# Kernel optimization log

Hardware: AMD Instinct MI355X
Metric: run time of the kernel (lower is better)

The kernel has to match this reference:

```python
import jax, jax.numpy as jnp
import numpy as np

POOL_H, POOL_W = 7, 7


def _crop_and_resize(fmap, boxes, box_idx, ph, pw):
    """TF tf.image.crop_and_resize (bilinear) for normalized boxes.
    fmap: [B,H,W,C], boxes: [M,4] (y1,x1,y2,x2), box_idx: [M] int32 -> [M,ph,pw,C]."""
    H, W = fmap.shape[1], fmap.shape[2]
    dt = fmap.dtype
    y1, x1, y2, x2 = jnp.split(boxes.astype(dt), 4, axis=1)  # each [M,1]
    gy = jnp.arange(ph, dtype=dt) / (ph - 1)
    gx = jnp.arange(pw, dtype=dt) / (pw - 1)
    ys = (y1 + (y2 - y1) * gy[None, :]) * (H - 1)  # [M,ph]
    xs = (x1 + (x2 - x1) * gx[None, :]) * (W - 1)  # [M,pw]
    y0 = jnp.clip(jnp.floor(ys), 0, H - 1).astype(jnp.int32)
    x0 = jnp.clip(jnp.floor(xs), 0, W - 1).astype(jnp.int32)
    y1i = jnp.minimum(y0 + 1, H - 1)
    x1i = jnp.minimum(x0 + 1, W - 1)
    ly = (ys - y0.astype(dt))[:, :, None, None]  # [M,ph,1,1]
    lx = (xs - x0.astype(dt))[:, None, :, None]  # [M,1,pw,1]
    b = box_idx[:, None, None]
    tl = fmap[b, y0[:, :, None], x0[:, None, :]]   # [M,ph,pw,C]
    tr = fmap[b, y0[:, :, None], x1i[:, None, :]]
    bl = fmap[b, y1i[:, :, None], x0[:, None, :]]
    br = fmap[b, y1i[:, :, None], x1i[:, None, :]]
    top = tl + (tr - tl) * lx
    bot = bl + (br - bl) * lx
    return top + (bot - top) * ly


def pyramid_roi_align(boxes, image_meta, feature_maps):
    B, N, _ = boxes.shape
    y1, x1, y2, x2 = jnp.split(boxes, 4, axis=2)
    h = y2 - y1
    w = x2 - x1
    image_shape = image_meta[0, 4:7]
    image_area = image_shape[0] * image_shape[1]
    roi_level = jnp.log2(jnp.sqrt(h * w) / (224.0 / jnp.sqrt(image_area)))
    roi_level = jnp.clip(4 + jnp.round(roi_level).astype(jnp.int32), 2, 5)
    roi_level = roi_level.reshape(B * N)  # squeeze axis 2 + flatten

    flat_boxes = boxes.reshape(B * N, 4)
    box_idx = jnp.repeat(jnp.arange(B, dtype=jnp.int32), N)
    C = feature_maps[0].shape[-1]
    pooled = jnp.zeros((B * N, POOL_H, POOL_W, C), dtype=feature_maps[0].dtype)
    # Equivalent to TF's gather/crop/sort-restore: each box pooled from its level.
    for i, level in enumerate(range(2, 6)):
        crop = _crop_and_resize(feature_maps[i], flat_boxes, box_idx, POOL_H, POOL_W)
        mask = (roi_level == level)[:, None, None, None]
        pooled = jnp.where(mask, crop, pooled)
    return pooled.reshape(B, N, POOL_H, POOL_W, C)


def setup_inputs() -> dict:
    key = jax.random.key(0)
    k1, k2, k3, k4, k5, k6, k7, k8 = jax.random.split(key, 8)
    B, N, C = 2, 1000, 256
    # boxes: normalized y1,x1,y2,x2 with sizes spanning all FPN levels
    sz = jax.random.uniform(k1, (B, N, 1), minval=0.02, maxval=0.8)
    yx1 = jax.random.uniform(k2, (B, N, 2)) * (1.0 - sz)
    boxes = jnp.concatenate([yx1[..., :1], yx1[..., 1:], yx1[..., :1] + sz, yx1[..., 1:] + sz], axis=2)
    # image_meta: image_shape (1024,1024,3) at indices 4:7
    meta = np.zeros((B, 93), dtype=np.float32)
    meta[:, 1:4] = [1024, 1024, 3]
    meta[:, 4:7] = [1024, 1024, 3]
    meta[:, 11] = 1.0
    return {
        "boxes": boxes.astype(jnp.float32),
        "image_meta": jnp.asarray(meta),
        "feat_p2": jax.random.normal(k3, (B, 256, 256, C), dtype=jnp.float32),
        "feat_p3": jax.random.normal(k4, (B, 128, 128, C), dtype=jnp.float32),
        "feat_p4": jax.random.normal(k5, (B, 64, 64, C), dtype=jnp.float32),
        "feat_p5": jax.random.normal(k6, (B, 32, 32, C), dtype=jnp.float32),
    }


def reference(boxes, image_meta, feat_p2, feat_p3, feat_p4, feat_p5):
    return pyramid_roi_align(boxes, image_meta, (feat_p2, feat_p3, feat_p4, feat_p5))
```

## Files before the change

### kernel.cpp

```cpp
#include <hip/hip_runtime.h>


__global__ __launch_bounds__(256) void roi_align_kernel(
    const float* __restrict__ boxes,
    const float* __restrict__ meta,
    const float* __restrict__ f2,
    const float* __restrict__ f3,
    const float* __restrict__ f4,
    const float* __restrict__ f5,
    float* __restrict__ out,
    int boxes_per_batch,
    long total4)
{
    long idx = (long)blockIdx.x * blockDim.x + threadIdx.x;
    if (idx >= total4) return;

    int c4  = (int)(idx & 63);
    long t  = idx >> 6;
    int p   = (int)(t % 49);
    int box = (int)(t / 49);
    int py = p / 7, px = p % 7;

    float by1 = boxes[4 * box + 0];
    float bx1 = boxes[4 * box + 1];
    float by2 = boxes[4 * box + 2];
    float bx2 = boxes[4 * box + 3];

    float h = by2 - by1, w = bx2 - bx1;
    float area  = meta[4] * meta[5];
    float scale = 224.0f / sqrtf(area);
    float rl    = log2f(sqrtf(h * w) / scale);
    int lvl = 4 + (int)rintf(rl);
    lvl = lvl < 2 ? 2 : (lvl > 5 ? 5 : lvl);
    int li = lvl - 2;
    const float* f = (li == 0) ? f2 : (li == 1) ? f3 : (li == 2) ? f4 : f5;
    int H = 256 >> li;

    int b = box / boxes_per_batch;

    float gy = (float)py / 6.0f;
    float gx = (float)px / 6.0f;
    float ys = (by1 + (by2 - by1) * gy) * (float)(H - 1);
    float xs = (bx1 + (bx2 - bx1) * gx) * (float)(H - 1);

    float fy0 = fminf(fmaxf(floorf(ys), 0.0f), (float)(H - 1));
    float fx0 = fminf(fmaxf(floorf(xs), 0.0f), (float)(H - 1));
    int y0 = (int)fy0, x0 = (int)fx0;
    int y1i = min(y0 + 1, H - 1);
    int x1i = min(x0 + 1, H - 1);
    float ly = ys - fy0;
    float lx = xs - fx0;

    const int C = 256;
    size_t row0 = ((size_t)b * H + y0)  * H;
    size_t row1 = ((size_t)b * H + y1i) * H;
    const float4* tl = (const float4*)(f + (row0 + x0)  * C) + c4;
    const float4* tr = (const float4*)(f + (row0 + x1i) * C) + c4;
    const float4* bl = (const float4*)(f + (row1 + x0)  * C) + c4;
    const float4* br = (const float4*)(f + (row1 + x1i) * C) + c4;

    float4 vtl = *tl, vtr = *tr, vbl = *bl, vbr = *br;
    float4 r;
    float top, bot;
    top = vtl.x + (vtr.x - vtl.x) * lx; bot = vbl.x + (vbr.x - vbl.x) * lx; r.x = top + (bot - top) * ly;
    top = vtl.y + (vtr.y - vtl.y) * lx; bot = vbl.y + (vbr.y - vbl.y) * lx; r.y = top + (bot - top) * ly;
    top = vtl.z + (vtr.z - vtl.z) * lx; bot = vbl.z + (vbr.z - vbl.z) * lx; r.z = top + (bot - top) * ly;
    top = vtl.w + (vtr.w - vtl.w) * lx; bot = vbl.w + (vbr.w - vbl.w) * lx; r.w = top + (bot - top) * ly;

    ((float4*)out)[idx] = r;
}

extern "C" void kernel_launch(void* const* d_in, const int* in_sizes, int n_in,
                              void* d_out, int out_size, void* d_ws, size_t ws_size,
                              hipStream_t stream) {
    const float* boxes = (const float*)d_in[0];
    const float* meta  = (const float*)d_in[1];
    const float* f2    = (const float*)d_in[2];
    const float* f3    = (const float*)d_in[3];
    const float* f4    = (const float*)d_in[4];
    const float* f5    = (const float*)d_in[5];
    float* out         = (float*)d_out;

    int n_boxes = in_sizes[0] / 4;
    int B       = in_sizes[2] / (256 * 256 * 256);
    int boxes_per_batch = n_boxes / B;

    long total4 = (long)n_boxes * 49 * 64;
    int blocks  = (int)((total4 + 255) / 256);
    roi_align_kernel<<<blocks, 256, 0, stream>>>(
        boxes, meta, f2, f3, f4, f5, out, boxes_per_batch, total4);
}
```

Measured before the change: 43.15 us.

## Split ROI align into per-box prep kernel and XCD-swizzled gather kernel

Adds a prep kernel that computes, per box, the pyramid level and the per-axis row/column offsets and interpolation weights into workspace. The gather kernel then reads these tables instead of recomputing log2/sqrt per thread. Each thread now handles two float4 channel chunks, output uses nontemporal stores, and block IDs are remapped so that contiguous work lands on the same XCD for L2 locality. The cost is an extra kernel launch and workspace traffic, and the new path depends on the workspace being large enough; otherwise it falls back to the old kernel.

```diff
diff --git a/kernel.cpp b/kernel.cpp
--- a/kernel.cpp
+++ b/kernel.cpp
@@ -1,5 +1,135 @@
 #include <hip/hip_runtime.h>
-
+#include <math.h>
+
+
+#define POOLN 7
+#define CCH 256
+
+typedef float f32x4 __attribute__((ext_vector_type(4)));
+
+struct __align__(16) AxisInfo { int r0; int r1; float l; int pad; };
+
+__global__ __launch_bounds__(64) void roi_prep_kernel(
+    const float* __restrict__ boxes,
+    const float* __restrict__ meta,
+    int* __restrict__ liArr,
+    AxisInfo* __restrict__ yinfo,
+    AxisInfo* __restrict__ xinfo,
+    int n_boxes, int boxes_per_batch)
+{
+    int tid = blockIdx.x * blockDim.x + threadIdx.x;
+    int box = tid / POOLN;
+    int j   = tid - box * POOLN;
+    if (box >= n_boxes) return;
+
+    float by1 = boxes[4 * box + 0];
+    float bx1 = boxes[4 * box + 1];
+    float by2 = boxes[4 * box + 2];
+    float bx2 = boxes[4 * box + 3];
+    float h = by2 - by1, w = bx2 - bx1;
+
+    float area  = meta[4] * meta[5];
+    float scale = 224.0f / sqrtf(area);
+    float rl    = log2f(sqrtf(h * w) / scale);
+    int lvl = 4 + (int)rintf(rl);
+    lvl = lvl < 2 ? 2 : (lvl > 5 ? 5 : lvl);
+    int li = lvl - 2;
+    int H  = 256 >> li;
+    if (j == 0) liArr[box] = li;
+
+    int b = box / boxes_per_batch;
+    float g = (float)j / 6.0f;
+    float hm1 = (float)(H - 1);
+
+    float ys  = (by1 + h * g) * hm1;
+    float fy0 = fminf(fmaxf(floorf(ys), 0.0f), hm1);
+    int y0  = (int)fy0;
+    int y1i = min(y0 + 1, H - 1);
+    AxisInfo yi;
+    yi.r0 = ((b * H + y0)  * H) * CCH;
+    yi.r1 = ((b * H + y1i) * H) * CCH;
+    yi.l  = ys - fy0;
+    yi.pad = 0;
+    yinfo[box * POOLN + j] = yi;
+
+    float xs  = (bx1 + w * g) * hm1;
+    float fx0 = fminf(fmaxf(floorf(xs), 0.0f), hm1);
+    int x0  = (int)fx0;
+    int x1i = min(x0 + 1, H - 1);
+    AxisInfo xi;
+    xi.r0 = x0  * CCH;
+    xi.r1 = x1i * CCH;
+    xi.l  = xs - fx0;
+    xi.pad = 0;
+    xinfo[box * POOLN + j] = xi;
+}
+
+__device__ __forceinline__ f32x4 bilerp4(f32x4 tl, f32x4 tr, f32x4 bl, f32x4 br,
+                                         float lx, float ly)
+{
+    f32x4 r;
+    float top, bot;
+    top = tl.x + (tr.x - tl.x) * lx; bot = bl.x + (br.x - bl.x) * lx; r.x = top + (bot - top) * ly;
+    top = tl.y + (tr.y - tl.y) * lx; bot = bl.y + (br.y - bl.y) * lx; r.y = top + (bot - top) * ly;
+    top = tl.z + (tr.z - tl.z) * lx; bot = bl.z + (br.z - bl.z) * lx; r.z = top + (bot - top) * ly;
+    top = tl.w + (tr.w - tl.w) * lx; bot = bl.w + (br.w - bl.w) * lx; r.w = top + (bot - top) * ly;
+    return r;
+}
+
+__global__ __launch_bounds__(256) void roi_gather_kernel(
+    const int* __restrict__ liArr,
+    const AxisInfo* __restrict__ yinfo,
+    const AxisInfo* __restrict__ xinfo,
+    const float* __restrict__ f2,
+    const float* __restrict__ f3,
+    const float* __restrict__ f4,
+    const float* __restrict__ f5,
+    float* __restrict__ out,
+    int q, int r, long total)
+{
+    int bid    = blockIdx.x;
+    int xcd    = bid & 7;
+    int within = bid >> 3;
+    int wg = (xcd < r ? xcd * (q + 1) : r * (q + 1) + (xcd - r) * q) + within;
+
+    long wid = (long)wg * 256 + threadIdx.x;
+    if (wid >= total) return;
+
+    int  c4  = (int)(wid & 31);
+    long t   = wid >> 5;
+    int  box = (int)(t / 49);
+    int  p   = (int)(t - (long)box * 49);
+    int  py  = (p * 37) >> 8;
+    int  px  = p - py * 7;
+
+    int li = liArr[box];
+    const float* f = (li == 0) ? f2 : (li == 1) ? f3 : (li == 2) ? f4 : f5;
+    AxisInfo yi = yinfo[box * POOLN + py];
+    AxisInfo xi = xinfo[box * POOLN + px];
+    float ly = yi.l, lx = xi.l;
+
+    int co = c4 * 4;
+    const float* ptl = f + yi.r0 + xi.r0 + co;
+    const float* ptr2= f + yi.r0 + xi.r1 + co;
+    const float* pbl = f + yi.r1 + xi.r0 + co;
+    const float* pbr = f + yi.r1 + xi.r1 + co;
+
+    f32x4 tlA = *(const f32x4*)ptl;
+    f32x4 trA = *(const f32x4*)ptr2;
+    f32x4 blA = *(const f32x4*)pbl;
+    f32x4 brA = *(const f32x4*)pbr;
+    f32x4 tlB = *(const f32x4*)(ptl + 128);
+    f32x4 trB = *(const f32x4*)(ptr2 + 128);
+    f32x4 blB = *(const f32x4*)(pbl + 128);
+    f32x4 brB = *(const f32x4*)(pbr + 128);
+
+    f32x4 rA = bilerp4(tlA, trA, blA, brA, lx, ly);
+    f32x4 rB = bilerp4(tlB, trB, blB, brB, lx, ly);
+
+    long obase = t * CCH + co;
+    __builtin_nontemporal_store(rA, (f32x4*)(out + obase));
+    __builtin_nontemporal_store(rB, (f32x4*)(out + obase + 128));
+}
 
 __global__ __launch_bounds__(256) void roi_align_kernel(
     const float* __restrict__ boxes,
@@ -51,23 +181,15 @@
     float ly = ys - fy0;
     float lx = xs - fx0;
 
-    const int C = 256;
     size_t row0 = ((size_t)b * H + y0)  * H;
     size_t row1 = ((size_t)b * H + y1i) * H;
-    const float4* tl = (const float4*)(f + (row0 + x0)  * C) + c4;
-    const float4* tr = (const float4*)(f + (row0 + x1i) * C) + c4;
-    const float4* bl = (const float4*)(f + (row1 + x0)  * C) + c4;
-    const float4* br = (const float4*)(f + (row1 + x1i) * C) + c4;
-
-    float4 vtl = *tl, vtr = *tr, vbl = *bl, vbr = *br;
-    float4 r;
-    float top, bot;
-    top = vtl.x + (vtr.x - vtl.x) * lx; bot = vbl.x + (vbr.x - vbl.x) * lx; r.x = top + (bot - top) * ly;
-    top = vtl.y + (vtr.y - vtl.y) * lx; bot = vbl.y + (vbr.y - vbl.y) * lx; r.y = top + (bot - top) * ly;
-    top = vtl.z + (vtr.z - vtl.z) * lx; bot = vbl.z + (vbr.z - vbl.z) * lx; r.z = top + (bot - top) * ly;
-    top = vtl.w + (vtr.w - vtl.w) * lx; bot = vbl.w + (vbr.w - vbl.w) * lx; r.w = top + (bot - top) * ly;
-
-    ((float4*)out)[idx] = r;
+    const f32x4* tl = (const f32x4*)(f + (row0 + x0)  * CCH) + c4;
+    const f32x4* tr = (const f32x4*)(f + (row0 + x1i) * CCH) + c4;
+    const f32x4* bl = (const f32x4*)(f + (row1 + x0)  * CCH) + c4;
+    const f32x4* br = (const f32x4*)(f + (row1 + x1i) * CCH) + c4;
+
+    f32x4 rr = bilerp4(*tl, *tr, *bl, *br, lx, ly);
+    ((f32x4*)out)[idx] = rr;
 }
 
 extern "C" void kernel_launch(void* const* d_in, const int* in_sizes, int n_in,
@@ -85,8 +207,28 @@
     int B       = in_sizes[2] / (256 * 256 * 256);
     int boxes_per_batch = n_boxes / B;
 
-    long total4 = (long)n_boxes * 49 * 64;
-    int blocks  = (int)((total4 + 255) / 256);
-    roi_align_kernel<<<blocks, 256, 0, stream>>>(
-        boxes, meta, f2, f3, f4, f5, out, boxes_per_batch, total4);
-}
+    size_t li_bytes   = 16384;
+    size_t axis_bytes = (size_t)n_boxes * POOLN * sizeof(AxisInfo);
+    size_t need = li_bytes + 2 * axis_bytes;
+
+    if (d_ws != nullptr && ws_size >= need) {
+        int*      liArr = (int*)d_ws;
+        AxisInfo* yinfo = (AxisInfo*)((char*)d_ws + li_bytes);
+        AxisInfo* xinfo = yinfo + (size_t)n_boxes * POOLN;
+
+        int prep_threads = n_boxes * POOLN;
+        roi_prep_kernel<<<(prep_threads + 63) / 64, 64, 0, stream>>>(
+            boxes, meta, liArr, yinfo, xinfo, n_boxes, boxes_per_batch);
+
+        long total = (long)n_boxes * 49 * 32;
+        int  nwg   = (int)((total + 255) / 256);
+        int  q = nwg >> 3, r = nwg & 7;
+        roi_gather_kernel<<<nwg, 256, 0, stream>>>(
+            liArr, yinfo, xinfo, f2, f3, f4, f5, out, q, r, total);
+    } else {
+        long total4 = (long)n_boxes * 49 * 64;
+        int  blocks = (int)((total4 + 255) / 256);
+        roi_align_kernel<<<blocks, 256, 0, stream>>>(
+            boxes, meta, f2, f3, f4, f5, out, boxes_per_batch, total4);
+    }
+}
```

Result: no change. 42.40 us (-1.7%).
